# Kernel tuning notes

Hardware: AMD Instinct MI355X
Metric: run time of the kernel (lower is better)

Reference implementation:

```python
import jax, jax.numpy as jnp
import numpy as np

B, N, D = 2, 2048, 1024
H, HD = 16, 64            # num_heads, head_dim
INNER = H * HD
EPS = 1e-5


def setup_inputs() -> dict:
    key = jax.random.key(0)
    k0, k1, k2, k3 = jax.random.split(key, 4)
    x = jax.random.normal(k0, (B, N, D), dtype=jnp.float32)
    attn_mask = jax.random.randint(k1, (B, N, N), 0, 2, dtype=jnp.int32)
    gamma = jnp.ones((D,), jnp.float32)
    beta = jnp.zeros((D,), jnp.float32)
    w_qkv = jax.random.normal(k2, (D, 3 * INNER), dtype=jnp.float32) * 0.02
    w_out = jax.random.normal(k3, (INNER, D), dtype=jnp.float32) * 0.02
    b_out = jnp.zeros((D,), jnp.float32)
    return {"x": x, "attn_mask": attn_mask, "gamma": gamma, "beta": beta,
            "w_qkv": w_qkv, "w_out": w_out, "b_out": b_out}


def _rope_tables(n):
    # RotaryEmbedding buffers: sin/cos of shape [n, HD//2]
    inv_freq = 1.0 / (10000.0 ** (jnp.arange(0, HD, 2, dtype=jnp.float32) / HD))
    pos = jnp.arange(n, dtype=jnp.float32)
    ang = pos[:, None] * inv_freq[None, :]          # [n, HD//2]
    return jnp.sin(ang), jnp.cos(ang)


def _apply_rope(t, sin, cos):
    # t: [B, H, N, HD]; sin/cos broadcast as [1, 1, N, HD//2]
    t1, t2 = t[..., : HD // 2], t[..., HD // 2:]
    return jnp.concatenate([t1 * cos - t2 * sin, t2 * cos + t1 * sin], axis=-1)


def reference(x, attn_mask, gamma, beta, w_qkv, w_out, b_out):
    b, n, _ = x.shape
    # LayerNorm
    mu = jnp.mean(x, axis=-1, keepdims=True)
    var = jnp.mean(jnp.square(x - mu), axis=-1, keepdims=True)
    xn = (x - mu) * jax.lax.rsqrt(var + EPS) * gamma + beta
    # QKV projection (no bias)
    qkv = xn @ w_qkv                                 # [B, N, 3*INNER]
    q, k, v = jnp.split(qkv, 3, axis=-1)
    def to_heads(t):
        return t.reshape(b, n, H, HD).transpose(0, 2, 1, 3)  # [B, H, N, HD]
    q, k, v = to_heads(q), to_heads(k), to_heads(v)
    sin, cos = _rope_tables(n)
    sin = sin[None, None]                            # [1,1,N,HD//2]
    cos = cos[None, None]
    q = _apply_rope(q, sin, cos)
    k = _apply_rope(k, sin, cos)
    scale = HD ** -0.5
    scores = jnp.einsum('bhid,bhjd->bhij', q, k) * scale
    mask = (attn_mask > 0)[:, None, :, :]            # [B,1,N,N]
    scores = jnp.where(mask, scores, -jnp.inf)
    probs = jax.nn.softmax(scores, axis=-1)
    probs = jnp.nan_to_num(probs, nan=0.0)           # rows fully masked -> 0
    out = jnp.einsum('bhij,bhjd->bhid', probs, v)    # [B,H,N,HD]
    out = out.transpose(0, 2, 1, 3).reshape(b, n, INNER)
    return out @ w_out + b_out
```

## Files before the change

### kernel.cpp

```cpp
#include <hip/hip_runtime.h>
#include <stdint.h>
#include <math.h>

#define B_ 2
#define N_ 2048
#define D_ 1024
#define H_ 16
#define HD_ 64
#define TOK (B_*N_)
#define INNER_ (H_*HD_)

typedef unsigned short u16;
typedef __attribute__((ext_vector_type(8))) short bf16x8;
typedef __attribute__((ext_vector_type(4))) float f32x4;

__device__ __forceinline__ float bf2f(u16 u) {
  union { uint32_t i; float f; } v; v.i = ((uint32_t)u) << 16; return v.f;
}
__device__ __forceinline__ u16 f2bf(float f) {
  union { uint32_t i; float f; } v; v.f = f;
  uint32_t r = ((v.i >> 16) & 1u) + 0x7fffu;
  return (u16)((v.i + r) >> 16);
}
__device__ __forceinline__ uint32_t pk_trunc(float a, float b) {
  return __builtin_amdgcn_perm(__float_as_uint(b), __float_as_uint(a), 0x07060302);
}
__device__ __forceinline__ uint32_t pk_rnd(float a, float b) {
  uint32_t ua = __float_as_uint(a) + 0x8000u;
  uint32_t ub = __float_as_uint(b) + 0x8000u;
  return __builtin_amdgcn_perm(ub, ua, 0x07060302);
}
__device__ __forceinline__ void gl_lds16(const void* g, void* l) {
  __builtin_amdgcn_global_load_lds(
      (const __attribute__((address_space(1))) uint32_t*)g,
      (__attribute__((address_space(3))) uint32_t*)l, 16, 0, 0);
}
__device__ __forceinline__ f32x4 mfma16(bf16x8 a, bf16x8 b, f32x4 c) {
  return __builtin_amdgcn_mfma_f32_16x16x32_bf16(a, b, c, 0, 0, 0);
}

__global__ void pack_mask(const int* __restrict__ mask, uint64_t* __restrict__ bits) {
  int t = threadIdx.x, lane = t & 63, w = t >> 6;
  int seg = blockIdx.x * 4 + w;
  int row = seg >> 3, s = seg & 7;
  const int* mp = mask + (size_t)row * 2048 + s * 256;
  int b = row >> 11, i = row & 2047;
  uint64_t* bp = bits + (size_t)b * 32 * 2048 + i;
  for (int j = 0; j < 4; j++) {
    int m = mp[j * 64 + lane];
    uint64_t bm = __ballot(m > 0);
    if (lane == 0) bp[(size_t)(s * 4 + j) * 2048] = bm;
  }
}

__global__ void rtab_kernel(float2* __restrict__ rtab) {
  int i = blockIdx.x * 256 + threadIdx.x;
  int pos = i >> 5, p = i & 31;
  float inv = exp2f(-(float)p * (13.287712379549449f / 32.0f));
  float sn, cs;
  sincosf((float)pos * inv, &sn, &cs);
  rtab[i] = make_float2(sn, cs);
}

__global__ void transpose_f2b(const float* __restrict__ in, u16* __restrict__ out,
                              int R, int C) {
  __shared__ u16 tile[64][65];
  int c0 = blockIdx.x * 64, r0 = blockIdx.y * 64;
  int t = threadIdx.x;
  int c = t & 63, r4 = t >> 6;
  for (int i = 0; i < 16; i++) {
    int r = r4 + i * 4;
    tile[c][r] = f2bf(in[(size_t)(r0 + r) * C + c0 + c]);
  }
  __syncthreads();
  int rr = t & 63, cc4 = t >> 6;
  for (int i = 0; i < 16; i++) {
    int cc = cc4 + i * 4;
    out[(size_t)(c0 + cc) * R + r0 + rr] = tile[cc][rr];
  }
}

__global__ void ln_kernel(const float* __restrict__ x, const float* __restrict__ gamma,
                          const float* __restrict__ beta, u16* __restrict__ xn) {
  int row = blockIdx.x, t = threadIdx.x;
  const float* xr = x + (size_t)row * D_;
  float4 u = *(const float4*)(xr + t * 4);
  float s = u.x + u.y + u.z + u.w;
  float ss = u.x * u.x + u.y * u.y + u.z * u.z + u.w * u.w;
  for (int off = 1; off < 64; off <<= 1) {
    s += __shfl_xor(s, off);
    ss += __shfl_xor(ss, off);
  }
  __shared__ float red[8];
  int wid = t >> 6, lane = t & 63;
  if (lane == 0) { red[wid] = s; red[wid + 4] = ss; }
  __syncthreads();
  s = red[0] + red[1] + red[2] + red[3];
  ss = red[4] + red[5] + red[6] + red[7];
  float mu = s * (1.0f / D_);
  float var = ss * (1.0f / D_) - mu * mu;
  float rinv = rsqrtf(var + 1e-5f);
  float4 g4 = *(const float4*)(gamma + t * 4);
  float4 b4 = *(const float4*)(beta + t * 4);
  ushort4 o;
  o.x = f2bf((u.x - mu) * rinv * g4.x + b4.x);
  o.y = f2bf((u.y - mu) * rinv * g4.y + b4.y);
  o.z = f2bf((u.z - mu) * rinv * g4.z + b4.z);
  o.w = f2bf((u.w - mu) * rinv * g4.w + b4.w);
  *(ushort4*)(xn + (size_t)row * D_ + t * 4) = o;
}

__global__ void gemm_qkv(const u16* __restrict__ A, const u16* __restrict__ Bt,
                         const float2* __restrict__ rtab,
                         u16* __restrict__ q, u16* __restrict__ k,
                         u16* __restrict__ vt) {
  const int K = 1024;
  __shared__ __align__(16) u16 As[128 * 64];
  __shared__ __align__(16) u16 Bs[128 * 64];
  const int t = threadIdx.x;
  const int lane = t & 63, wid = t >> 6;
  const int m0 = blockIdx.y * 128, n0 = blockIdx.x * 128;
  const int wm = (wid >> 1) * 64, wn = (wid & 1) * 64;
  const int l15 = lane & 15, quad = lane >> 4;

  f32x4 acc[4][4];
  const f32x4 zf = {0.f, 0.f, 0.f, 0.f};
  for (int i = 0; i < 4; i++) for (int j = 0; j < 4; j++) acc[i][j] = zf;

  for (int kb = 0; kb < K; kb += 64) {
    for (int i = 0; i < 4; i++) {
      int e = i * 256 + t;
      int row = e >> 3, gs = e & 7;
      int g = gs ^ (row & 7);
      gl_lds16(A + (size_t)(m0 + row) * K + kb + g * 8, &As[e * 8]);
      gl_lds16(Bt + (size_t)(n0 + row) * K + kb + g * 8, &Bs[e * 8]);
    }
    __syncthreads();
    bf16x8 af[4][2], bfr[4][2];
    for (int mt = 0; mt < 4; mt++)
      for (int kc = 0; kc < 2; kc++) {
        int row = wm + mt * 16 + l15;
        int gs = (kc * 4 + quad) ^ (row & 7);
        af[mt][kc] = *(const bf16x8*)&As[row * 64 + gs * 8];
      }
    for (int nt = 0; nt < 4; nt++)
      for (int kc = 0; kc < 2; kc++) {
        int row = wn + nt * 16 + l15;
        int gs = (kc * 4 + quad) ^ (row & 7);
        bfr[nt][kc] = *(const bf16x8*)&Bs[row * 64 + gs * 8];
      }
    for (int mt = 0; mt < 4; mt++)
      for (int nt = 0; nt < 4; nt++)
        for (int kc = 0; kc < 2; kc++)
          acc[mt][nt] = mfma16(af[mt][kc], bfr[nt][kc], acc[mt][nt]);
    __syncthreads();
  }

  const int sec = n0 >> 10;
  const int h = ((n0 & 1023) >> 6) + (wn >> 6);
  if (sec < 2) {
    u16* dst = sec ? k : q;
    const float scale = sec ? 1.0f : 0.125f * 1.4426950408889634f;
    for (int mt = 0; mt < 4; mt++)
      for (int r = 0; r < 4; r++) {
        int row = m0 + wm + mt * 16 + quad * 4 + r;
        int b = row >> 11, pos = row & 2047;
        float2 c0 = rtab[pos * 32 + l15];
        float2 c1 = rtab[pos * 32 + 16 + l15];
        float a0 = acc[mt][0][r], a1 = acc[mt][1][r];
        float a2 = acc[mt][2][r], a3 = acc[mt][3][r];
        float o0 = (a0 * c0.y - a2 * c0.x) * scale;
        float o2 = (a2 * c0.y + a0 * c0.x) * scale;
        float o1 = (a1 * c1.y - a3 * c1.x) * scale;
        float o3 = (a3 * c1.y + a1 * c1.x) * scale;
        size_t base = ((size_t)(b * 16 + h) * 2048 + pos) * 64;
        dst[base + l15]      = f2bf(o0);
        dst[base + 16 + l15] = f2bf(o1);
        dst[base + 32 + l15] = f2bf(o2);
        dst[base + 48 + l15] = f2bf(o3);
      }
  } else {
    for (int mt = 0; mt < 4; mt++) {
      int u = (wm + mt * 16) >> 4;
      int c = (u >> 1) & 1, hi = u & 1;
      int rowb = m0 + (u >> 2) * 64;
      int b = rowb >> 11, nb = rowb & 2047;
      int slot = nb + c * 32 + quad * 8 + hi * 4;
      for (int nt = 0; nt < 4; nt++) {
        int d = nt * 16 + l15;
        size_t base = ((size_t)(b * 16 + h) * 64 + d) * 2048 + slot;
        uint2 o;
        o.x = pk_rnd(acc[mt][nt][0], acc[mt][nt][1]);
        o.y = pk_rnd(acc[mt][nt][2], acc[mt][nt][3]);
        *(uint2*)&vt[base] = o;
      }
    }
  }
}

__global__ void gemm_out(const u16* __restrict__ A, const u16* __restrict__ Bt,
                         float* __restrict__ C, const float* __restrict__ bias) {
  const int N = 1024, K = 1024;
  __shared__ __align__(16) u16 As[2][128 * 64];
  __shared__ __align__(16) u16 Bs[2][128 * 64];
  const int t = threadIdx.x;
  const int lane = t & 63, wid = t >> 6;
  const int m0 = blockIdx.y * 128, n0 = blockIdx.x * 128;
  const int wm = (wid >> 1) * 64, wn = (wid & 1) * 64;
  const int l15 = lane & 15, quad = lane >> 4;

  f32x4 acc[4][4];
  const f32x4 zf = {0.f, 0.f, 0.f, 0.f};
  for (int i = 0; i < 4; i++) for (int j = 0; j < 4; j++) acc[i][j] = zf;

  for (int i = 0; i < 4; i++) {
    int e = i * 256 + t;
    int row = e >> 3, gs = e & 7, g = gs ^ (row & 7);
    gl_lds16(A + (size_t)(m0 + row) * K + g * 8, &As[0][e * 8]);
    gl_lds16(Bt + (size_t)(n0 + row) * K + g * 8, &Bs[0][e * 8]);
  }
  for (int ki = 0; ki < 16; ki++) {
    int cur = ki & 1;
    __syncthreads();
    if (ki + 1 < 16) {
      int nxt = cur ^ 1, kb = (ki + 1) * 64;
      for (int i = 0; i < 4; i++) {
        int e = i * 256 + t;
        int row = e >> 3, gs = e & 7, g = gs ^ (row & 7);
        gl_lds16(A + (size_t)(m0 + row) * K + kb + g * 8, &As[nxt][e * 8]);
        gl_lds16(Bt + (size_t)(n0 + row) * K + kb + g * 8, &Bs[nxt][e * 8]);
      }
    }
    bf16x8 af[4][2], bfr[4][2];
    for (int mt = 0; mt < 4; mt++)
      for (int kc = 0; kc < 2; kc++) {
        int row = wm + mt * 16 + l15;
        int gs = (kc * 4 + quad) ^ (row & 7);
        af[mt][kc] = *(const bf16x8*)&As[cur][row * 64 + gs * 8];
      }
    for (int nt = 0; nt < 4; nt++)
      for (int kc = 0; kc < 2; kc++) {
        int row = wn + nt * 16 + l15;
        int gs = (kc * 4 + quad) ^ (row & 7);
        bfr[nt][kc] = *(const bf16x8*)&Bs[cur][row * 64 + gs * 8];
      }
    for (int mt = 0; mt < 4; mt++)
      for (int nt = 0; nt < 4; nt++)
        for (int kc = 0; kc < 2; kc++)
          acc[mt][nt] = mfma16(af[mt][kc], bfr[nt][kc], acc[mt][nt]);
  }
  for (int mt = 0; mt < 4; mt++)
    for (int nt = 0; nt < 4; nt++)
      for (int r = 0; r < 4; r++) {
        int row = m0 + wm + mt * 16 + quad * 4 + r;
        int col = n0 + wn + nt * 16 + l15;
        C[(size_t)row * N + col] = acc[mt][nt][r] + bias[col];
      }
}

__global__ __launch_bounds__(256, 4)
void attn_kernel(const u16* __restrict__ q, const u16* __restrict__ k,
                 const u16* __restrict__ vt, const uint64_t* __restrict__ bitsT,
                 u16* __restrict__ out) {
  int blk = blockIdx.x;
  int qt = blk & 31;
  int bh = blk >> 5;
  int b = bh >> 4, h = bh & 15;
  int q0 = qt * 64;
  int t = threadIdx.x, lane = t & 63, w = t >> 6;
  int l15 = lane & 15, quad = lane >> 4;

  __shared__ __align__(16) u16 sQ[64 * 64];
  __shared__ __align__(16) u16 sK[2][64 * 64];
  __shared__ __align__(16) u16 sV[2][64 * 64];

  {
    int e0 = t, e1 = 256 + t;
    int r0 = e0 >> 3, g0 = (e0 & 7) ^ (r0 & 7);
    int r1 = e1 >> 3, g1 = (e1 & 7) ^ (r1 & 7);
    gl_lds16(q + ((size_t)bh * 2048 + q0 + r0) * 64 + g0 * 8, &sQ[e0 * 8]);
    gl_lds16(q + ((size_t)bh * 2048 + q0 + r1) * 64 + g1 * 8, &sQ[e1 * 8]);
    gl_lds16(k + ((size_t)bh * 2048 + r0) * 64 + g0 * 8, &sK[0][e0 * 8]);
    gl_lds16(k + ((size_t)bh * 2048 + r1) * 64 + g1 * 8, &sK[0][e1 * 8]);
    gl_lds16(vt + ((size_t)bh * 64 + r0) * 2048 + g0 * 8, &sV[0][e0 * 8]);
    gl_lds16(vt + ((size_t)bh * 64 + r1) * 2048 + g1 * 8, &sV[0][e1 * 8]);
  }
  __syncthreads();

  bf16x8 bq[2];
  {
    int row = w * 16 + l15;
    for (int kc = 0; kc < 2; kc++) {
      int gs = (kc * 4 + quad) ^ (row & 7);
      bq[kc] = *(const bf16x8*)&sQ[row * 64 + gs * 8];
    }
  }

  const f32x4 zf = {0.f, 0.f, 0.f, 0.f};
  float l_i = 0.f;
  f32x4 acc_o[4];
  for (int dt = 0; dt < 4; dt++) acc_o[dt] = zf;
  const int qrow = q0 + w * 16 + l15;

  #pragma unroll 2
  for (int j64 = 0; j64 < 32; j64++) {
    if (j64) __syncthreads();
    int cur = j64 & 1;
    if (j64 + 1 < 32) {
      int nxt = cur ^ 1, j0n = (j64 + 1) * 64;
      int e0 = t, e1 = 256 + t;
      int r0 = e0 >> 3, g0 = (e0 & 7) ^ (r0 & 7);
      int r1 = e1 >> 3, g1 = (e1 & 7) ^ (r1 & 7);
      gl_lds16(k + ((size_t)bh * 2048 + j0n + r0) * 64 + g0 * 8, &sK[nxt][e0 * 8]);
      gl_lds16(k + ((size_t)bh * 2048 + j0n + r1) * 64 + g1 * 8, &sK[nxt][e1 * 8]);
      gl_lds16(vt + ((size_t)bh * 64 + r0) * 2048 + j0n + g0 * 8, &sV[nxt][e0 * 8]);
      gl_lds16(vt + ((size_t)bh * 64 + r1) * 2048 + j0n + g1 * 8, &sV[nxt][e1 * 8]);
    }
    const u16* sKc = sK[cur];
    const u16* sVc = sV[cur];

    uint64_t word = bitsT[((size_t)(b * 32 + j64)) * 2048 + qrow];
    uint64_t sh = word >> (quad * 4);
    uint32_t mlo = (uint32_t)sh, mhi = (uint32_t)(sh >> 32);

    float p[16];
    {
      f32x4 st[4];
      for (int jt = 0; jt < 4; jt++) {
        st[jt] = zf;
        int row = jt * 16 + l15;
        for (int kc = 0; kc < 2; kc++) {
          int gs = (kc * 4 + quad) ^ (row & 7);
          bf16x8 ak = *(const bf16x8*)&sKc[row * 64 + gs * 8];
          st[jt] = mfma16(ak, bq[kc], st[jt]);
        }
      }
      for (int jt = 0; jt < 4; jt++) {
        uint32_t mw = (jt & 2) ? mhi : mlo;
        int base = (jt & 1) * 16;
        for (int r = 0; r < 4; r++) {
          bool on = (mw >> (base + r)) & 1u;
          float e = exp2f(st[jt][r]);
          p[jt * 4 + r] = on ? e : 0.f;
        }
      }
    }
    float rsum = 0.f;
    for (int i = 0; i < 16; i++) rsum += p[i];
    rsum += __shfl_xor(rsum, 16);
    rsum += __shfl_xor(rsum, 32);
    l_i += rsum;

    for (int c = 0; c < 2; c++) {
      union { bf16x8 v; uint32_t d[4]; } bp;
      bp.d[0] = pk_trunc(p[(2 * c) * 4 + 0], p[(2 * c) * 4 + 1]);
      bp.d[1] = pk_trunc(p[(2 * c) * 4 + 2], p[(2 * c) * 4 + 3]);
      bp.d[2] = pk_trunc(p[(2 * c + 1) * 4 + 0], p[(2 * c + 1) * 4 + 1]);
      bp.d[3] = pk_trunc(p[(2 * c + 1) * 4 + 2], p[(2 * c + 1) * 4 + 3]);
      for (int dt = 0; dt < 4; dt++) {
        int drow = dt * 16 + l15;
        int gpos = (4 * c + quad) ^ (drow & 7);
        bf16x8 av = *(const bf16x8*)&sVc[drow * 64 + gpos * 8];
        acc_o[dt] = mfma16(av, bp.v, acc_o[dt]);
      }
    }
  }
  float rl = (l_i > 0.f) ? 1.0f / l_i : 0.f;
  size_t obase = ((size_t)b * 2048 + qrow) * 1024 + h * 64;
  for (int dt = 0; dt < 4; dt++) {
    ushort4 o;
    o.x = f2bf(acc_o[dt][0] * rl);
    o.y = f2bf(acc_o[dt][1] * rl);
    o.z = f2bf(acc_o[dt][2] * rl);
    o.w = f2bf(acc_o[dt][3] * rl);
    *(ushort4*)&out[obase + dt * 16 + quad * 4] = o;
  }
}

extern "C" void kernel_launch(void* const* d_in, const int* in_sizes, int n_in,
                              void* d_out, int out_size, void* d_ws, size_t ws_size,
                              hipStream_t stream) {
  const float* x = (const float*)d_in[0];
  const int* mask = (const int*)d_in[1];
  const float* gamma = (const float*)d_in[2];
  const float* beta = (const float*)d_in[3];
  const float* wqkv = (const float*)d_in[4];
  const float* wout = (const float*)d_in[5];
  const float* bout = (const float*)d_in[6];
  float* out = (float*)d_out;

  uint8_t* ws = (uint8_t*)d_ws;
  size_t o = 0;
  uint64_t* mbits = (uint64_t*)(ws + o); o += (size_t)TOK * 32 * 8;
  u16* wqkvT = (u16*)(ws + o); o += (size_t)3 * INNER_ * D_ * 2;
  u16* woutT = (u16*)(ws + o); o += (size_t)INNER_ * D_ * 2;
  u16* xn    = (u16*)(ws + o); o += (size_t)TOK * D_ * 2;
  u16* qb    = (u16*)(ws + o); o += (size_t)TOK * INNER_ * 2;
  u16* kb    = (u16*)(ws + o); o += (size_t)TOK * INNER_ * 2;
  u16* vtb   = (u16*)(ws + o); o += (size_t)TOK * INNER_ * 2;
  u16* ao    = (u16*)(ws + o); o += (size_t)TOK * INNER_ * 2;
  float2* rtab = (float2*)(ws + o); o += (size_t)2048 * 32 * 8;

  pack_mask<<<8192, 256, 0, stream>>>(mask, mbits);
  rtab_kernel<<<256, 256, 0, stream>>>(rtab);
  transpose_f2b<<<dim3(3 * INNER_ / 64, D_ / 64), 256, 0, stream>>>(wqkv, wqkvT, D_, 3 * INNER_);
  transpose_f2b<<<dim3(D_ / 64, INNER_ / 64), 256, 0, stream>>>(wout, woutT, INNER_, D_);
  ln_kernel<<<TOK, 256, 0, stream>>>(x, gamma, beta, xn);
  gemm_qkv<<<dim3(3 * INNER_ / 128, TOK / 128), 256, 0, stream>>>(xn, wqkvT, rtab, qb, kb, vtb);
  attn_kernel<<<B_ * H_ * (N_ / 64), 256, 0, stream>>>(qb, kb, vtb, mbits, ao);
  gemm_out<<<dim3(D_ / 128, TOK / 128), 256, 0, stream>>>(ao, woutT, out, bout);
}
```

Before: 247.2 us.

## Switch attention to 32x32 MFMA with 128-row query tiles and shrink out-GEMM tiles

Result: no change. 250.0 us (+1.1%).

```diff
diff --git a/kernel.cpp b/kernel.cpp
--- a/kernel.cpp
+++ b/kernel.cpp
@@ -13,6 +13,7 @@
 typedef unsigned short u16;
 typedef __attribute__((ext_vector_type(8))) short bf16x8;
 typedef __attribute__((ext_vector_type(4))) float f32x4;
+typedef __attribute__((ext_vector_type(16))) float f32x16;
 
 __device__ __forceinline__ float bf2f(u16 u) {
   union { uint32_t i; float f; } v; v.i = ((uint32_t)u) << 16; return v.f;
@@ -37,6 +38,9 @@
 }
 __device__ __forceinline__ f32x4 mfma16(bf16x8 a, bf16x8 b, f32x4 c) {
   return __builtin_amdgcn_mfma_f32_16x16x32_bf16(a, b, c, 0, 0, 0);
+}
+__device__ __forceinline__ f32x16 mfma32(bf16x8 a, bf16x8 b, f32x16 c) {
+  return __builtin_amdgcn_mfma_f32_32x32x16_bf16(a, b, c, 0, 0, 0);
 }
 
 __global__ void pack_mask(const int* __restrict__ mask, uint64_t* __restrict__ bits) {
@@ -181,14 +185,12 @@
       }
   } else {
     for (int mt = 0; mt < 4; mt++) {
-      int u = (wm + mt * 16) >> 4;
-      int c = (u >> 1) & 1, hi = u & 1;
-      int rowb = m0 + (u >> 2) * 64;
-      int b = rowb >> 11, nb = rowb & 2047;
-      int slot = nb + c * 32 + quad * 8 + hi * 4;
+      int tb = m0 + wm + mt * 16;
+      int bb = tb >> 11, nb = tb & 2047;
+      int slot = nb + (quad & 1) * 8 + (quad >> 1) * 4;
       for (int nt = 0; nt < 4; nt++) {
         int d = nt * 16 + l15;
-        size_t base = ((size_t)(b * 16 + h) * 64 + d) * 2048 + slot;
+        size_t base = ((size_t)(bb * 16 + h) * 64 + d) * 2048 + slot;
         uint2 o;
         o.x = pk_rnd(acc[mt][nt][0], acc[mt][nt][1]);
         o.y = pk_rnd(acc[mt][nt][2], acc[mt][nt][3]);
@@ -201,38 +203,48 @@
 __global__ void gemm_out(const u16* __restrict__ A, const u16* __restrict__ Bt,
                          float* __restrict__ C, const float* __restrict__ bias) {
   const int N = 1024, K = 1024;
-  __shared__ __align__(16) u16 As[2][128 * 64];
+  __shared__ __align__(16) u16 As[2][64 * 64];
   __shared__ __align__(16) u16 Bs[2][128 * 64];
   const int t = threadIdx.x;
   const int lane = t & 63, wid = t >> 6;
-  const int m0 = blockIdx.y * 128, n0 = blockIdx.x * 128;
-  const int wm = (wid >> 1) * 64, wn = (wid & 1) * 64;
+  const int m0 = blockIdx.y * 64, n0 = blockIdx.x * 128;
+  const int wm = (wid >> 1) * 32, wn = (wid & 1) * 64;
   const int l15 = lane & 15, quad = lane >> 4;
 
-  f32x4 acc[4][4];
+  f32x4 acc[2][4];
   const f32x4 zf = {0.f, 0.f, 0.f, 0.f};
-  for (int i = 0; i < 4; i++) for (int j = 0; j < 4; j++) acc[i][j] = zf;
-
-  for (int i = 0; i < 4; i++) {
-    int e = i * 256 + t;
-    int row = e >> 3, gs = e & 7, g = gs ^ (row & 7);
-    gl_lds16(A + (size_t)(m0 + row) * K + g * 8, &As[0][e * 8]);
-    gl_lds16(Bt + (size_t)(n0 + row) * K + g * 8, &Bs[0][e * 8]);
+  for (int i = 0; i < 2; i++) for (int j = 0; j < 4; j++) acc[i][j] = zf;
+
+  {
+    for (int i = 0; i < 2; i++) {
+      int e = i * 256 + t;
+      int row = e >> 3, gs = e & 7, g = gs ^ (row & 7);
+      gl_lds16(A + (size_t)(m0 + row) * K + g * 8, &As[0][e * 8]);
+    }
+    for (int i = 0; i < 4; i++) {
+      int e = i * 256 + t;
+      int row = e >> 3, gs = e & 7, g = gs ^ (row & 7);
+      gl_lds16(Bt + (size_t)(n0 + row) * K + g * 8, &Bs[0][e * 8]);
+    }
   }
   for (int ki = 0; ki < 16; ki++) {
     int cur = ki & 1;
     __syncthreads();
     if (ki + 1 < 16) {
       int nxt = cur ^ 1, kb = (ki + 1) * 64;
+      for (int i = 0; i < 2; i++) {
+        int e = i * 256 + t;
+        int row = e >> 3, gs = e & 7, g = gs ^ (row & 7);
+        gl_lds16(A + (size_t)(m0 + row) * K + kb + g * 8, &As[nxt][e * 8]);
+      }
       for (int i = 0; i < 4; i++) {
         int e = i * 256 + t;
         int row = e >> 3, gs = e & 7, g = gs ^ (row & 7);
-        gl_lds16(A + (size_t)(m0 + row) * K + kb + g * 8, &As[nxt][e * 8]);
         gl_lds16(Bt + (size_t)(n0 + row) * K + kb + g * 8, &Bs[nxt][e * 8]);
       }
     }
-    bf16x8 af[4][2], bfr[4][2];
-    for (int mt = 0; mt < 4; mt++)
+    bf16x8 af[2][2], bfr[4][2];
+    for (int mt = 0; mt < 2; mt++)
       for (int kc = 0; kc < 2; kc++) {
         int row = wm + mt * 16 + l15;
         int gs = (kc * 4 + quad) ^ (row & 7);
@@ -244,12 +256,12 @@
         int gs = (kc * 4 + quad) ^ (row & 7);
         bfr[nt][kc] = *(const bf16x8*)&Bs[cur][row * 64 + gs * 8];
       }
-    for (int mt = 0; mt < 4; mt++)
+    for (int mt = 0; mt < 2; mt++)
       for (int nt = 0; nt < 4; nt++)
         for (int kc = 0; kc < 2; kc++)
           acc[mt][nt] = mfma16(af[mt][kc], bfr[nt][kc], acc[mt][nt]);
   }
-  for (int mt = 0; mt < 4; mt++)
+  for (int mt = 0; mt < 2; mt++)
     for (int nt = 0; nt < 4; nt++)
       for (int r = 0; r < 4; r++) {
         int row = m0 + wm + mt * 16 + quad * 4 + r;
@@ -258,123 +270,115 @@
       }
 }
 
-__global__ __launch_bounds__(256, 4)
-void attn_kernel(const u16* __restrict__ q, const u16* __restrict__ k,
-                 const u16* __restrict__ vt, const uint64_t* __restrict__ bitsT,
-                 u16* __restrict__ out) {
+__global__ void attn_kernel(const u16* __restrict__ q, const u16* __restrict__ k,
+                            const u16* __restrict__ vt, const uint64_t* __restrict__ bitsT,
+                            u16* __restrict__ out) {
   int blk = blockIdx.x;
-  int qt = blk & 31;
-  int bh = blk >> 5;
+  int qt = blk & 15;
+  int bh = blk >> 4;
   int b = bh >> 4, h = bh & 15;
-  int q0 = qt * 64;
+  int q0 = qt * 128;
   int t = threadIdx.x, lane = t & 63, w = t >> 6;
-  int l15 = lane & 15, quad = lane >> 4;
-
-  __shared__ __align__(16) u16 sQ[64 * 64];
+  int l31 = lane & 31, hi = lane >> 5;
+
+  __shared__ __align__(16) u16 sQ[128 * 64];
   __shared__ __align__(16) u16 sK[2][64 * 64];
   __shared__ __align__(16) u16 sV[2][64 * 64];
 
-  {
-    int e0 = t, e1 = 256 + t;
-    int r0 = e0 >> 3, g0 = (e0 & 7) ^ (r0 & 7);
-    int r1 = e1 >> 3, g1 = (e1 & 7) ^ (r1 & 7);
-    gl_lds16(q + ((size_t)bh * 2048 + q0 + r0) * 64 + g0 * 8, &sQ[e0 * 8]);
-    gl_lds16(q + ((size_t)bh * 2048 + q0 + r1) * 64 + g1 * 8, &sQ[e1 * 8]);
-    gl_lds16(k + ((size_t)bh * 2048 + r0) * 64 + g0 * 8, &sK[0][e0 * 8]);
-    gl_lds16(k + ((size_t)bh * 2048 + r1) * 64 + g1 * 8, &sK[0][e1 * 8]);
-    gl_lds16(vt + ((size_t)bh * 64 + r0) * 2048 + g0 * 8, &sV[0][e0 * 8]);
-    gl_lds16(vt + ((size_t)bh * 64 + r1) * 2048 + g1 * 8, &sV[0][e1 * 8]);
+  for (int i = 0; i < 4; i++) {
+    int e = i * 256 + t;
+    int row = e >> 3, g = (e & 7) ^ (row & 7);
+    gl_lds16(q + ((size_t)bh * 2048 + q0 + row) * 64 + g * 8, &sQ[e * 8]);
+  }
+  for (int i = 0; i < 2; i++) {
+    int e = i * 256 + t;
+    int row = e >> 3, g = (e & 7) ^ (row & 7);
+    gl_lds16(k + ((size_t)bh * 2048 + row) * 64 + g * 8, &sK[0][e * 8]);
+    gl_lds16(vt + ((size_t)bh * 64 + row) * 2048 + g * 8, &sV[0][e * 8]);
   }
   __syncthreads();
 
-  bf16x8 bq[2];
-  {
-    int row = w * 16 + l15;
-    for (int kc = 0; kc < 2; kc++) {
-      int gs = (kc * 4 + quad) ^ (row & 7);
-      bq[kc] = *(const bf16x8*)&sQ[row * 64 + gs * 8];
-    }
-  }
-
-  const f32x4 zf = {0.f, 0.f, 0.f, 0.f};
+  const int qrow_l = w * 32 + l31;
+  bf16x8 bq[4];
+  for (int kc = 0; kc < 4; kc++) {
+    int gs = (kc * 2 + hi) ^ (qrow_l & 7);
+    bq[kc] = *(const bf16x8*)&sQ[qrow_l * 64 + gs * 8];
+  }
+
   float l_i = 0.f;
-  f32x4 acc_o[4];
-  for (int dt = 0; dt < 4; dt++) acc_o[dt] = zf;
-  const int qrow = q0 + w * 16 + l15;
-
-  #pragma unroll 2
+  f32x16 occ[2];
+  for (int dt = 0; dt < 2; dt++)
+    for (int i = 0; i < 16; i++) occ[dt][i] = 0.f;
+  const int qrow = q0 + qrow_l;
+
   for (int j64 = 0; j64 < 32; j64++) {
     if (j64) __syncthreads();
     int cur = j64 & 1;
     if (j64 + 1 < 32) {
       int nxt = cur ^ 1, j0n = (j64 + 1) * 64;
-      int e0 = t, e1 = 256 + t;
-      int r0 = e0 >> 3, g0 = (e0 & 7) ^ (r0 & 7);
-      int r1 = e1 >> 3, g1 = (e1 & 7) ^ (r1 & 7);
-      gl_lds16(k + ((size_t)bh * 2048 + j0n + r0) * 64 + g0 * 8, &sK[nxt][e0 * 8]);
-      gl_lds16(k + ((size_t)bh * 2048 + j0n + r1) * 64 + g1 * 8, &sK[nxt][e1 * 8]);
-      gl_lds16(vt + ((size_t)bh * 64 + r0) * 2048 + j0n + g0 * 8, &sV[nxt][e0 * 8]);
-      gl_lds16(vt + ((size_t)bh * 64 + r1) * 2048 + j0n + g1 * 8, &sV[nxt][e1 * 8]);
+      for (int i = 0; i < 2; i++) {
+        int e = i * 256 + t;
+        int row = e >> 3, g = (e & 7) ^ (row & 7);
+        gl_lds16(k + ((size_t)bh * 2048 + j0n + row) * 64 + g * 8, &sK[nxt][e * 8]);
+        gl_lds16(vt + ((size_t)bh * 64 + row) * 2048 + j0n + g * 8, &sV[nxt][e * 8]);
+      }
     }
     const u16* sKc = sK[cur];
     const u16* sVc = sV[cur];
 
     uint64_t word = bitsT[((size_t)(b * 32 + j64)) * 2048 + qrow];
-    uint64_t sh = word >> (quad * 4);
-    uint32_t mlo = (uint32_t)sh, mhi = (uint32_t)(sh >> 32);
-
-    float p[16];
-    {
-      f32x4 st[4];
-      for (int jt = 0; jt < 4; jt++) {
-        st[jt] = zf;
-        int row = jt * 16 + l15;
-        for (int kc = 0; kc < 2; kc++) {
-          int gs = (kc * 4 + quad) ^ (row & 7);
-          bf16x8 ak = *(const bf16x8*)&sKc[row * 64 + gs * 8];
-          st[jt] = mfma16(ak, bq[kc], st[jt]);
-        }
-      }
-      for (int jt = 0; jt < 4; jt++) {
-        uint32_t mw = (jt & 2) ? mhi : mlo;
-        int base = (jt & 1) * 16;
-        for (int r = 0; r < 4; r++) {
-          bool on = (mw >> (base + r)) & 1u;
-          float e = exp2f(st[jt][r]);
-          p[jt * 4 + r] = on ? e : 0.f;
-        }
+
+    float p[32];
+    #pragma unroll
+    for (int jt = 0; jt < 2; jt++) {
+      f32x16 st;
+      for (int i = 0; i < 16; i++) st[i] = 0.f;
+      for (int kc = 0; kc < 4; kc++) {
+        int row = jt * 32 + l31;
+        int gs = (kc * 2 + hi) ^ (row & 7);
+        bf16x8 ak = *(const bf16x8*)&sKc[row * 64 + gs * 8];
+        st = mfma32(ak, bq[kc], st);
+      }
+      uint32_t mw = (uint32_t)(word >> (jt * 32)) >> (4 * hi);
+      #pragma unroll
+      for (int reg = 0; reg < 16; reg++) {
+        int bitpos = (reg & 3) + 8 * (reg >> 2);
+        bool on = (mw >> bitpos) & 1u;
+        p[jt * 16 + reg] = on ? exp2f(st[reg]) : 0.f;
       }
     }
     float rsum = 0.f;
-    for (int i = 0; i < 16; i++) rsum += p[i];
-    rsum += __shfl_xor(rsum, 16);
+    for (int i = 0; i < 32; i++) rsum += p[i];
     rsum += __shfl_xor(rsum, 32);
     l_i += rsum;
 
-    for (int c = 0; c < 2; c++) {
+    #pragma unroll
+    for (int c = 0; c < 4; c++) {
+      const float* pc = &p[(c >> 1) * 16 + (c & 1) * 8];
       union { bf16x8 v; uint32_t d[4]; } bp;
-      bp.d[0] = pk_trunc(p[(2 * c) * 4 + 0], p[(2 * c) * 4 + 1]);
-      bp.d[1] = pk_trunc(p[(2 * c) * 4 + 2], p[(2 * c) * 4 + 3]);
-      bp.d[2] = pk_trunc(p[(2 * c + 1) * 4 + 0], p[(2 * c + 1) * 4 + 1]);
-      bp.d[3] = pk_trunc(p[(2 * c + 1) * 4 + 2], p[(2 * c + 1) * 4 + 3]);
-      for (int dt = 0; dt < 4; dt++) {
-        int drow = dt * 16 + l15;
-        int gpos = (4 * c + quad) ^ (drow & 7);
-        bf16x8 av = *(const bf16x8*)&sVc[drow * 64 + gpos * 8];
-        acc_o[dt] = mfma16(av, bp.v, acc_o[dt]);
+      bp.d[0] = pk_trunc(pc[0], pc[1]);
+      bp.d[1] = pk_trunc(pc[2], pc[3]);
+      bp.d[2] = pk_trunc(pc[4], pc[5]);
+      bp.d[3] = pk_trunc(pc[6], pc[7]);
+      for (int dt = 0; dt < 2; dt++) {
+        int drow = dt * 32 + l31;
+        int gs = (c * 2 + hi) ^ (drow & 7);
+        bf16x8 av = *(const bf16x8*)&sVc[drow * 64 + gs * 8];
+        occ[dt] = mfma32(av, bp.v, occ[dt]);
       }
     }
   }
   float rl = (l_i > 0.f) ? 1.0f / l_i : 0.f;
   size_t obase = ((size_t)b * 2048 + qrow) * 1024 + h * 64;
-  for (int dt = 0; dt < 4; dt++) {
-    ushort4 o;
-    o.x = f2bf(acc_o[dt][0] * rl);
-    o.y = f2bf(acc_o[dt][1] * rl);
-    o.z = f2bf(acc_o[dt][2] * rl);
-    o.w = f2bf(acc_o[dt][3] * rl);
-    *(ushort4*)&out[obase + dt * 16 + quad * 4] = o;
-  }
+  for (int dt = 0; dt < 2; dt++)
+    #pragma unroll
+    for (int g = 0; g < 4; g++) {
+      int d0 = dt * 32 + g * 8 + hi * 4;
+      uint2 ov;
+      ov.x = pk_rnd(occ[dt][g * 4 + 0] * rl, occ[dt][g * 4 + 1] * rl);
+      ov.y = pk_rnd(occ[dt][g * 4 + 2] * rl, occ[dt][g * 4 + 3] * rl);
+      *(uint2*)&out[obase + d0] = ov;
+    }
 }
 
 extern "C" void kernel_launch(void* const* d_in, const int* in_sizes, int n_in,
@@ -407,6 +411,6 @@
   transpose_f2b<<<dim3(D_ / 64, INNER_ / 64), 256, 0, stream>>>(wout, woutT, INNER_, D_);
   ln_kernel<<<TOK, 256, 0, stream>>>(x, gamma, beta, xn);
   gemm_qkv<<<dim3(3 * INNER_ / 128, TOK / 128), 256, 0, stream>>>(xn, wqkvT, rtab, qb, kb, vtb);
-  attn_kernel<<<B_ * H_ * (N_ / 64), 256, 0, stream>>>(qb, kb, vtb, mbits, ao);
-  gemm_out<<<dim3(D_ / 128, TOK / 128), 256, 0, stream>>>(ao, woutT, out, bout);
-}
+  attn_kernel<<<B_ * H_ * (N_ / 128), 256, 0, stream>>>(qb, kb, vtb, mbits, ao);
+  gemm_out<<<dim3(D_ / 128, TOK / 64), 256, 0, stream>>>(ao, woutT, out, bout);
+}
```
